# Kernel tuning notes

Measured on AMD Instinct MI355X. Metric: run time of the kernel, lower is better.

## Reference

```python
import jax, jax.numpy as jnp
from jax import lax
import numpy as np

NUM_HEADS = 8
KW = 3  # window kernel size

def _avgpool3(x):
    # x: [B,C,H,W]; AvgPool2d(3,1,1) with count_include_pad=True -> sum/9
    s = lax.reduce_window(x, 0.0, lax.add, (1, 1, KW, KW), (1, 1, 1, 1),
                          ((0, 0), (0, 0), (1, 1), (1, 1)))
    return s / (KW * KW)

def _unfold3(y):
    # y: [B,h,w,C] -> [B,h,w,9,C]; patch index ordered row-major (kh,kw)
    B, h, w, C = y.shape
    yp = jnp.pad(y, ((0, 0), (1, 1), (1, 1), (0, 0)))
    return jnp.stack([yp[:, i:i + h, j:j + w, :]
                      for i in range(KW) for j in range(KW)], axis=3)

def setup_inputs():
    key = jax.random.key(0)
    ks = jax.random.split(key, 9)
    B, C, H, W = 8, 256, 64, 64
    sd = 0.02
    return {
        "x": jax.random.normal(ks[0], (B, C, H, W), jnp.float32),
        "W_qkv": jax.random.normal(ks[1], (4 * C, C), jnp.float32) * sd,
        "b_qkv": jnp.zeros((4 * C,), jnp.float32),
        "W1": jax.random.normal(ks[2], (C // 2, C), jnp.float32) * sd,
        "b1": jnp.zeros((C // 2,), jnp.float32),
        "W2": jax.random.normal(ks[3], (C, C // 2), jnp.float32) * sd,
        "b2": jnp.zeros((C,), jnp.float32),
        "Wp": jax.random.normal(ks[4], (C, C), jnp.float32) * sd,
        "bp": jnp.zeros((C,), jnp.float32),
    }

def reference(x, W_qkv, b_qkv, W1, b1, W2, b2, Wp, bp):
    B, C, H, W = x.shape
    nH = NUM_HEADS
    hd = C // nH
    scale = hd ** -0.5
    # avg pool (stride 1 keeps spatial dims), to channels-last
    y = _avgpool3(x).transpose(0, 2, 3, 1)                 # [B,h,w,C]
    qkv = y @ W_qkv.T + b_qkv                              # [B,h,w,4C]
    qkv = qkv.reshape(B, H, W, C, 4)
    q, k, v, chans = qkv[..., 0], qkv[..., 1], qkv[..., 2], qkv[..., 3]
    # channel gate
    g = jax.nn.sigmoid(jax.nn.relu(chans @ W1.T + b1) @ W2.T + b2)  # [B,h,w,C]
    # local window attention: each query attends to its 3x3 neighborhood
    qh = q.reshape(B, H, W, nH, hd)                        # [B,h,w,n,d]
    kp = _unfold3(k).reshape(B, H, W, KW * KW, nH, hd)     # [B,h,w,9,n,d]
    vp = _unfold3(v).reshape(B, H, W, KW * KW, nH, hd)
    attn = jnp.einsum('bhwnd,bhwknd->bhwnk', qh, kp) * scale
    attn = jax.nn.softmax(attn, axis=-1)
    out = jnp.einsum('bhwnk,bhwknd->bhwnd', attn, vp).reshape(B, H, W, C)
    out = out * g + out
    out = out @ Wp.T + bp
    return out.transpose(0, 3, 1, 2)                       # [B,C,H,W]
```

## Files before the change

### kernel.cpp

```cpp
#include <hip/hip_runtime.h>
#include <stdint.h>

typedef __bf16    bf16x8 __attribute__((ext_vector_type(8)));
typedef float     f32x4  __attribute__((ext_vector_type(4)));
typedef uint32_t  u32x4  __attribute__((ext_vector_type(4)));
typedef uint32_t  u32x2  __attribute__((ext_vector_type(2)));

#define MFMA(a,b,c) __builtin_amdgcn_mfma_f32_16x16x32_bf16((a),(b),(c),0,0,0)

__device__ __align__(16) uint16_t g_y [8*64*64*256];
__device__ __align__(16) uint16_t g_wpk[393216];

#define WQF 0
#define WKF 65536
#define WVF 131072
#define WCF 196608
#define W1F 262144
#define W2F 294912
#define WPF 327680

static __device__ __forceinline__ float b2f(uint32_t u){ return __builtin_bit_cast(float, u<<16); }
static __device__ __forceinline__ uint32_t f2b(float f){
  uint32_t x = __builtin_bit_cast(uint32_t, f);
  return (x + 0x7fffu + ((x>>16)&1u)) >> 16;
}

__global__ __launch_bounds__(512) void kprep(const float* __restrict__ x,
    const float* __restrict__ Wqkv, const float* __restrict__ W1,
    const float* __restrict__ W2, const float* __restrict__ Wp){
  int t = threadIdx.x;
  int bid = blockIdx.x;
  if (bid < 1024){
    __shared__ __align__(16) uint16_t sm[3*128*82];
    uint32_t* smw = (uint32_t*)sm;
    int b = bid >> 7, h = (bid >> 1) & 63, ch = (bid & 1) << 7;
    for (int i=t; i<384; i+=512){
      int base = i*41;
      smw[base+3]  = 0;
      smw[base+36] = 0;
    }
    if (h==0 || h==63){
      int hh = (h==0) ? 0 : 2;
      for (int i=t; i<5248; i+=512) smw[hh*5248 + i] = 0;
    }
    #pragma unroll
    for (int i=0;i<12;i++){
      int id = t + 512*i;
      int w4 = id&15, c = (id>>4)&127, hh = id>>11;
      int gy = h - 1 + hh;
      if ((unsigned)gy < 64u){
        f32x4 ld = *(const f32x4*)&x[(((b*256+ch+c)*64+gy)*64) + w4*4];
        int wb = (((hh*128+c)*82 + 8 + w4*4) >> 1);
        smw[wb+0] = f2b(ld[0]) | (f2b(ld[1])<<16);
        smw[wb+1] = f2b(ld[2]) | (f2b(ld[3])<<16);
      }
    }
    __syncthreads();
    int c = t & 127, wsel = t >> 7;
    int r0 = c*82, r1 = r0 + 128*82, r2 = r1 + 128*82;
    int w0 = wsel*16;
    float csp = b2f(sm[r0+w0+7]) + b2f(sm[r1+w0+7]) + b2f(sm[r2+w0+7]);
    float csc = b2f(sm[r0+w0+8]) + b2f(sm[r1+w0+8]) + b2f(sm[r2+w0+8]);
    uint16_t* dst = g_y + ((b*64+h)*64)*256 + ch + c;
    for (int j2=0;j2<16;j2++){
      int w = w0 + j2;
      float csn = b2f(sm[r0+w+9]) + b2f(sm[r1+w+9]) + b2f(sm[r2+w+9]);
      float yv = (csp + csc + csn) * (1.0f/9.0f);
      dst[w*256] = (uint16_t)f2b(yv);
      csp = csc; csc = csn;
    }
  } else {
    int idx = (bid - 1024)*512 + t;
    int j = idx & 7, lane = (idx>>3)&63;
    int n16 = lane & 15, q4 = lane>>4;
    float v;
    if (idx < 262144){
      int tt = idx >> 16, l = idx & 65535;
      int s = (l>>9)&7, nt = l>>12;
      v = Wqkv[(4*(nt*16+n16) + tt)*256 + s*32 + q4*8 + j];
    } else if (idx < 294912){
      int l = idx - 262144;
      int s = (l>>9)&7, nt = l>>12;
      v = W1[(nt*16+n16)*256 + s*32 + q4*8 + j];
    } else if (idx < 327680){
      int l = idx - 294912;
      int s = (l>>9)&3, nt = l>>11;
      v = W2[(nt*16+n16)*128 + s*32 + q4*8 + j];
    } else {
      int l = idx - 327680;
      int s = (l>>9)&7, nt = l>>12;
      v = Wp[(nt*16+n16)*256 + s*32 + q4*8 + j];
    }
    g_wpk[idx] = (uint16_t)f2b(v);
  }
}

#define YSTR  264
#define HSTR  136
#define K2_QS 15840
#define K2_KS 20192
#define K2_VS 28352
#define MCH   0
#define MHS   8448
#define MAO   15840
#define MAOSTR 266
#define MAOT  15840
#define MTSTR 36
__global__ __launch_bounds__(512,4) void kattn(const float* __restrict__ bqkv,
    const float* __restrict__ b1, const float* __restrict__ b2v,
    const float* __restrict__ bp, float* __restrict__ out){
  __shared__ __align__(16) uint16_t sm[36512];
  int t = threadIdx.x;
  int lane = t & 63, wave = t >> 6;
  int n16 = lane & 15, quad = lane >> 4;
  int bid = blockIdx.x;
  int bb = bid >> 7, ty = (bid >> 3) & 15, tx = bid & 7;

  uint32_t opk[2][8];
  uint32_t chp[16];

  #pragma unroll
  for (int i=0;i<4;i++){
    int id = t + 512*i;
    if (id < 1920){
      int hp = id >> 5, c8 = id & 31;
      int py = hp/10, px = hp - py*10;
      int gy = ty*4 + py - 1, gx = tx*8 + px - 1;
      u32x4 ld = {0,0,0,0};
      if ((unsigned)gy<64u && (unsigned)gx<64u)
        ld = *(const u32x4*)&g_y[((bb*64+gy)*64+gx)*256 + c8*8];
      *(u32x4*)&sm[hp*YSTR + c8*8] = ld;
    }
  }
  __syncthreads();

  #pragma unroll
  for (int hf=0; hf<2; hf++){
    {
      int ntg = hf*8 + wave;
      bf16x8 Bq[8];
      #pragma unroll
      for (int s=0;s<8;s++) Bq[s] = *(const bf16x8*)&g_wpk[WQF + ((ntg*8+s)*64+lane)*8];
      float bq = bqkv[4*(ntg*16+n16) + 0];
      int colB = wave*16;
      #pragma unroll
      for (int mt=0; mt<2; mt++){
        f32x4 a = {0.f,0.f,0.f,0.f};
        int m = mt*16 + n16;
        int hrow = 10*(m>>3) + (m&7) + 11;
        #pragma unroll
        for (int s=0;s<8;s++){
          bf16x8 A = *(const bf16x8*)&sm[hrow*YSTR + s*32 + quad*8];
          a = MFMA(A, Bq[s], a);
        }
        #pragma unroll
        for (int r=0;r<4;r++){
          int row = mt*16 + quad*4 + r;
          sm[K2_QS + row*HSTR + colB + n16] = (uint16_t)f2b(a[r] + bq);
        }
      }
    }
    __syncthreads();
    {
      int ntg = hf*8 + wave;
      bf16x8 Bk[8], Bv[8];
      #pragma unroll
      for (int s=0;s<8;s++){
        Bk[s] = *(const bf16x8*)&g_wpk[WKF + ((ntg*8+s)*64+lane)*8];
        Bv[s] = *(const bf16x8*)&g_wpk[WVF + ((ntg*8+s)*64+lane)*8];
      }
      float bk = bqkv[4*(ntg*16+n16) + 1];
      float bv = bqkv[4*(ntg*16+n16) + 2];
      int colB = wave*16;
      #pragma unroll
      for (int mt=0; mt<4; mt++){
        f32x4 ak = {0.f,0.f,0.f,0.f}, av = {0.f,0.f,0.f,0.f};
        int m = mt*16 + n16;
        int mr = (m < 60) ? m : 59;
        #pragma unroll
        for (int s=0;s<8;s++){
          bf16x8 A = *(const bf16x8*)&sm[mr*YSTR + s*32 + quad*8];
          ak = MFMA(A, Bk[s], ak);
          av = MFMA(A, Bv[s], av);
        }
        #pragma unroll
        for (int r=0;r<4;r++){
          int row = mt*16 + quad*4 + r;
          if (row < 60){
            int py = row/10, px = row - py*10;
            int gy = ty*4 + py - 1, gx = tx*8 + px - 1;
            bool ok = ((unsigned)gy<64u) && ((unsigned)gx<64u);
            float vk = ok ? ak[r] + bk : 0.f;
            float vv = ok ? av[r] + bv : 0.f;
            sm[K2_KS + row*HSTR + colB + n16] = (uint16_t)f2b(vk);
            sm[K2_VS + row*HSTR + colB + n16] = (uint16_t)f2b(vv);
          }
        }
      }
    }
    __syncthreads();
    if (wave < 4){
      int p = lane & 31, half = lane >> 5;
      int cb = wave*32 + half*16;
      const uint16_t* qp = &sm[K2_QS + p*HSTR + cb];
      u32x4 qa = *(const u32x4*)qp;
      u32x4 qb = *(const u32x4*)(qp+8);
      float qv[16];
      #pragma unroll
      for (int i=0;i<4;i++){
        qv[2*i]    = b2f(qa[i]&0xffffu); qv[2*i+1]   = b2f(qa[i]>>16);
        qv[8+2*i]  = b2f(qb[i]&0xffffu); qv[8+2*i+1] = b2f(qb[i]>>16);
      }
      int hb = 10*(p>>3) + (p&7) + 11;
      const int off[9] = {-11,-10,-9,-1,0,1,9,10,11};
      float sc[9];
      #pragma unroll
      for (int nb=0;nb<9;nb++){
        const uint16_t* kp = &sm[K2_KS + (hb+off[nb])*HSTR + cb];
        u32x4 ka = *(const u32x4*)kp;
        u32x4 kb = *(const u32x4*)(kp+8);
        float s = 0.f;
        #pragma unroll
        for (int i=0;i<4;i++){
          s += qv[2*i]*b2f(ka[i]&0xffffu)   + qv[2*i+1]*b2f(ka[i]>>16);
          s += qv[8+2*i]*b2f(kb[i]&0xffffu) + qv[8+2*i+1]*b2f(kb[i]>>16);
        }
        s += __shfl_xor(s, 32);
        sc[nb] = s * 0.17677669529663687f;
      }
      float mx = sc[0];
      #pragma unroll
      for (int nb=1;nb<9;nb++) mx = fmaxf(mx, sc[nb]);
      float l = 0.f;
      #pragma unroll
      for (int nb=0;nb<9;nb++){ sc[nb] = __expf(sc[nb]-mx); l += sc[nb]; }
      float inv = 1.f / l;
      float o[16];
      #pragma unroll
      for (int i=0;i<16;i++) o[i]=0.f;
      #pragma unroll
      for (int nb=0;nb<9;nb++){
        float wgt = sc[nb]*inv;
        const uint16_t* vp = &sm[K2_VS + (hb+off[nb])*HSTR + cb];
        u32x4 va = *(const u32x4*)vp;
        u32x4 vb = *(const u32x4*)(vp+8);
        #pragma unroll
        for (int i=0;i<4;i++){
          o[2*i]    += wgt*b2f(va[i]&0xffffu); o[2*i+1]   += wgt*b2f(va[i]>>16);
          o[8+2*i]  += wgt*b2f(vb[i]&0xffffu); o[8+2*i+1] += wgt*b2f(vb[i]>>16);
        }
      }
      #pragma unroll
      for (int i=0;i<8;i++) opk[hf][i] = f2b(o[2*i]) | (f2b(o[2*i+1])<<16);
    } else if (hf == 0){
      #pragma unroll
      for (int jj=0;jj<4;jj++){
        int ntg = (wave-4)*4 + jj;
        bf16x8 Bc[8];
        #pragma unroll
        for (int s=0;s<8;s++) Bc[s] = *(const bf16x8*)&g_wpk[WCF + ((ntg*8+s)*64+lane)*8];
        float bc = bqkv[4*(ntg*16+n16) + 3];
        #pragma unroll
        for (int mt=0; mt<2; mt++){
          f32x4 a = {0.f,0.f,0.f,0.f};
          int m = mt*16 + n16;
          int hrow = 10*(m>>3) + (m&7) + 11;
          #pragma unroll
          for (int s=0;s<8;s++){
            bf16x8 A = *(const bf16x8*)&sm[hrow*YSTR + s*32 + quad*8];
            a = MFMA(A, Bc[s], a);
          }
          chp[(jj*2+mt)*2+0] = f2b(a[0]+bc) | (f2b(a[1]+bc)<<16);
          chp[(jj*2+mt)*2+1] = f2b(a[2]+bc) | (f2b(a[3]+bc)<<16);
        }
      }
    } else {
      #pragma unroll
      for (int jj=0;jj<4;jj++){
        int ntg = (wave-4)*4 + jj;
        int col = ntg*16 + n16;
        #pragma unroll
        for (int mt=0;mt<2;mt++){
          #pragma unroll
          for (int r2=0;r2<2;r2++){
            uint32_t v = chp[(jj*2+mt)*2+r2];
            int row = mt*16 + quad*4 + r2*2;
            sm[MCH + row*264 + col]     = (uint16_t)(v & 0xffffu);
            sm[MCH + (row+1)*264 + col] = (uint16_t)(v >> 16);
          }
        }
      }
    }
    __syncthreads();
  }
  if (wave < 4){
    int p = lane & 31, half = lane >> 5;
    int cb = wave*32 + half*16;
    #pragma unroll
    for (int hf=0;hf<2;hf++)
      #pragma unroll
      for (int i=0;i<8;i++)
        *(uint32_t*)&sm[MAO + p*MAOSTR + hf*128 + cb + 2*i] = opk[hf][i];
  }
  {
    int ntg = wave;
    bf16x8 Bf[8];
    #pragma unroll
    for (int s=0;s<8;s++) Bf[s] = *(const bf16x8*)&g_wpk[W1F + ((ntg*8+s)*64+lane)*8];
    float bs = b1[ntg*16+n16];
    int colB = wave*16;
    #pragma unroll
    for (int mt=0;mt<2;mt++){
      f32x4 a = {0.f,0.f,0.f,0.f};
      #pragma unroll
      for (int s=0;s<8;s++){
        bf16x8 A = *(const bf16x8*)&sm[MCH + (mt*16+n16)*264 + s*32 + quad*8];
        a = MFMA(A, Bf[s], a);
      }
      #pragma unroll
      for (int r=0;r<4;r++){
        int row = mt*16 + quad*4 + r;
        sm[MHS + row*HSTR + colB + n16] = (uint16_t)f2b(fmaxf(a[r]+bs, 0.f));
      }
    }
  }
  __syncthreads();
  #pragma unroll
  for (int jj=0;jj<2;jj++){
    int ntg = wave*2 + jj;
    bf16x8 Bf[4];
    #pragma unroll
    for (int s=0;s<4;s++) Bf[s] = *(const bf16x8*)&g_wpk[W2F + ((ntg*4+s)*64+lane)*8];
    float bs = b2v[ntg*16+n16];
    int colB = ntg*16;
    #pragma unroll
    for (int mt=0;mt<2;mt++){
      f32x4 a = {0.f,0.f,0.f,0.f};
      #pragma unroll
      for (int s=0;s<4;s++){
        bf16x8 A = *(const bf16x8*)&sm[MHS + (mt*16+n16)*HSTR + s*32 + quad*8];
        a = MFMA(A, Bf[s], a);
      }
      #pragma unroll
      for (int r=0;r<4;r++){
        int row = mt*16 + quad*4 + r;
        float gg = 1.f/(1.f+__expf(-(a[r] + bs)));
        float ao = b2f((uint32_t)sm[MAO + row*MAOSTR + colB + n16]);
        sm[MCH + row*264 + colB + n16] = (uint16_t)f2b(ao*(1.f+gg));
      }
    }
  }
  __syncthreads();
  #pragma unroll
  for (int jj=0;jj<2;jj++){
    int ntg = wave*2 + jj;
    bf16x8 Bf[8];
    #pragma unroll
    for (int s=0;s<8;s++) Bf[s] = *(const bf16x8*)&g_wpk[WPF + ((ntg*8+s)*64+lane)*8];
    float bs = bp[ntg*16+n16];
    int colB = ntg*16;
    #pragma unroll
    for (int mt=0;mt<2;mt++){
      f32x4 a = {0.f,0.f,0.f,0.f};
      #pragma unroll
      for (int s=0;s<8;s++){
        bf16x8 A = *(const bf16x8*)&sm[MCH + (mt*16+n16)*264 + s*32 + quad*8];
        a = MFMA(A, Bf[s], a);
      }
      uint32_t lo = f2b(a[0]+bs) | (f2b(a[1]+bs)<<16);
      uint32_t hi = f2b(a[2]+bs) | (f2b(a[3]+bs)<<16);
      int col = colB + n16, row0 = mt*16 + quad*4;
      u32x2 pk = {lo, hi};
      *(u32x2*)&sm[MAOT + col*MTSTR + row0] = pk;
    }
  }
  __syncthreads();
  #pragma unroll
  for (int i=0;i<4;i++){
    int idx = t + 512*i;
    int ix4 = idx&1, iy = (idx>>1)&3, c = idx>>3;
    int p0 = iy*8 + ix4*4;
    u32x2 pk = *(const u32x2*)&sm[MAOT + c*MTSTR + p0];
    f32x4 stv;
    stv[0] = b2f(pk[0]&0xffffu); stv[1] = b2f(pk[0]>>16);
    stv[2] = b2f(pk[1]&0xffffu); stv[3] = b2f(pk[1]>>16);
    *(f32x4*)&out[(((bb*256+c)*64) + ty*4+iy)*64 + tx*8 + ix4*4] = stv;
  }
}

extern "C" void kernel_launch(void* const* d_in, const int* in_sizes, int n_in,
                              void* d_out, int out_size, void* d_ws, size_t ws_size,
                              hipStream_t stream){
  (void)in_sizes; (void)n_in; (void)d_ws; (void)ws_size; (void)out_size;
  const float* x    = (const float*)d_in[0];
  const float* Wqkv = (const float*)d_in[1];
  const float* bqkv = (const float*)d_in[2];
  const float* W1   = (const float*)d_in[3];
  const float* b1   = (const float*)d_in[4];
  const float* W2   = (const float*)d_in[5];
  const float* b2   = (const float*)d_in[6];
  const float* Wp   = (const float*)d_in[7];
  const float* bp   = (const float*)d_in[8];
  kprep<<<dim3(1792), dim3(512), 0, stream>>>(x, Wqkv, W1, W2, Wp);
  kattn<<<dim3(1024), dim3(512), 0, stream>>>(bqkv, b1, b2, bp, (float*)d_out);
}
```

Before: 186.1 us.

## Rebalance attention kernel schedule so waves overlap Q projection with attention

Restructures the fused attention kernel. All waves now compute the first-half Q and the channel-gate projection together up front. Waves 4-7 then compute the second-half Q into a separate buffer while waves 0-3 run the first attention pass, and the second attention pass overlaps with the channel scatter into shared memory. The conversion to bf16 now uses the native __bf16 cast, and bf16 unpacking uses a mask instead of a shift. The W2 and Wp GEMMs are restructured to reuse their A fragments across two output tiles. Shared memory grows to hold a second Q buffer, which may reduce occupancy, and the idle-wave imbalance in the attention phase is reduced.

```diff
diff --git a/kernel.cpp b/kernel.cpp
--- a/kernel.cpp
+++ b/kernel.cpp
@@ -20,9 +20,13 @@
 #define WPF 327680
 
 static __device__ __forceinline__ float b2f(uint32_t u){ return __builtin_bit_cast(float, u<<16); }
-static __device__ __forceinline__ uint32_t f2b(float f){
-  uint32_t x = __builtin_bit_cast(uint32_t, f);
-  return (x + 0x7fffu + ((x>>16)&1u)) >> 16;
+static __device__ __forceinline__ float blo(uint32_t u){ return __builtin_bit_cast(float, u<<16); }
+static __device__ __forceinline__ float bhi(uint32_t u){ return __builtin_bit_cast(float, u & 0xffff0000u); }
+static __device__ __forceinline__ uint16_t f2bn(float f){
+  return __builtin_bit_cast(uint16_t, (__bf16)f);
+}
+static __device__ __forceinline__ uint32_t pk2(float x, float y){
+  return (uint32_t)f2bn(x) | ((uint32_t)f2bn(y) << 16);
 }
 
 __global__ __launch_bounds__(512) void kprep(const float* __restrict__ x,
@@ -51,8 +55,8 @@
       if ((unsigned)gy < 64u){
         f32x4 ld = *(const f32x4*)&x[(((b*256+ch+c)*64+gy)*64) + w4*4];
         int wb = (((hh*128+c)*82 + 8 + w4*4) >> 1);
-        smw[wb+0] = f2b(ld[0]) | (f2b(ld[1])<<16);
-        smw[wb+1] = f2b(ld[2]) | (f2b(ld[3])<<16);
+        smw[wb+0] = pk2(ld[0], ld[1]);
+        smw[wb+1] = pk2(ld[2], ld[3]);
       }
     }
     __syncthreads();
@@ -66,7 +70,7 @@
       int w = w0 + j2;
       float csn = b2f(sm[r0+w+9]) + b2f(sm[r1+w+9]) + b2f(sm[r2+w+9]);
       float yv = (csp + csc + csn) * (1.0f/9.0f);
-      dst[w*256] = (uint16_t)f2b(yv);
+      dst[w*256] = f2bn(yv);
       csp = csc; csc = csn;
     }
   } else {
@@ -91,33 +95,94 @@
       int s = (l>>9)&7, nt = l>>12;
       v = Wp[(nt*16+n16)*256 + s*32 + q4*8 + j];
     }
-    g_wpk[idx] = (uint16_t)f2b(v);
+    g_wpk[idx] = f2bn(v);
   }
 }
 
 #define YSTR  264
+#define QA    15840
+#define QB    20192
+#define KS    24544
+#define VS    32704
 #define HSTR  136
-#define K2_QS 15840
-#define K2_KS 20192
-#define K2_VS 28352
 #define MCH   0
 #define MHS   8448
 #define MAO   15840
 #define MAOSTR 266
 #define MAOT  15840
 #define MTSTR 36
+
+static __device__ __forceinline__ void attn_pass(const uint16_t* sm, int qbase,
+    int lane, int wave, uint32_t* opk){
+  int p = lane & 31, half = lane >> 5;
+  int cb = wave*32 + half*16;
+  const uint16_t* qp = &sm[qbase + p*HSTR + cb];
+  u32x4 qa = *(const u32x4*)qp;
+  u32x4 qb = *(const u32x4*)(qp+8);
+  float qv[16];
+  #pragma unroll
+  for (int i=0;i<4;i++){
+    qv[2*i]    = blo(qa[i]); qv[2*i+1]   = bhi(qa[i]);
+    qv[8+2*i]  = blo(qb[i]); qv[8+2*i+1] = bhi(qb[i]);
+  }
+  int hb = 10*(p>>3) + (p&7) + 11;
+  const int off[9] = {-11,-10,-9,-1,0,1,9,10,11};
+  float sc[9];
+  #pragma unroll
+  for (int nb=0;nb<9;nb++){
+    const uint16_t* kp = &sm[KS + (hb+off[nb])*HSTR + cb];
+    u32x4 ka = *(const u32x4*)kp;
+    u32x4 kb = *(const u32x4*)(kp+8);
+    float s = 0.f;
+    #pragma unroll
+    for (int i=0;i<4;i++){
+      s += qv[2*i]*blo(ka[i])   + qv[2*i+1]*bhi(ka[i]);
+      s += qv[8+2*i]*blo(kb[i]) + qv[8+2*i+1]*bhi(kb[i]);
+    }
+    s += __shfl_xor(s, 32);
+    sc[nb] = s * 0.17677669529663687f;
+  }
+  float mx = sc[0];
+  #pragma unroll
+  for (int nb=1;nb<9;nb++) mx = fmaxf(mx, sc[nb]);
+  float l = 0.f;
+  #pragma unroll
+  for (int nb=0;nb<9;nb++){ sc[nb] = __expf(sc[nb]-mx); l += sc[nb]; }
+  float inv = 1.f / l;
+  float o[16];
+  #pragma unroll
+  for (int i=0;i<16;i++) o[i]=0.f;
+  #pragma unroll
+  for (int nb=0;nb<9;nb++){
+    float wgt = sc[nb]*inv;
+    const uint16_t* vp = &sm[VS + (hb+off[nb])*HSTR + cb];
+    u32x4 va = *(const u32x4*)vp;
+    u32x4 vb = *(const u32x4*)(vp+8);
+    #pragma unroll
+    for (int i=0;i<4;i++){
+      o[2*i]    += wgt*blo(va[i]); o[2*i+1]   += wgt*bhi(va[i]);
+      o[8+2*i]  += wgt*blo(vb[i]); o[8+2*i+1] += wgt*bhi(vb[i]);
+    }
+  }
+  #pragma unroll
+  for (int i=0;i<8;i++) opk[i] = pk2(o[2*i], o[2*i+1]);
+}
+
 __global__ __launch_bounds__(512,4) void kattn(const float* __restrict__ bqkv,
     const float* __restrict__ b1, const float* __restrict__ b2v,
     const float* __restrict__ bp, float* __restrict__ out){
-  __shared__ __align__(16) uint16_t sm[36512];
+  __shared__ __align__(16) uint16_t sm[40864];
   int t = threadIdx.x;
   int lane = t & 63, wave = t >> 6;
   int n16 = lane & 15, quad = lane >> 4;
   int bid = blockIdx.x;
   int bb = bid >> 7, ty = (bid >> 3) & 15, tx = bid & 7;
 
-  uint32_t opk[2][8];
-  uint32_t chp[16];
+  uint32_t opk0[8], opk1[8];
+  uint32_t chp[8];
+
+  int hrow0 = 10*(n16>>3) + (n16&7) + 11;
+  int hrow1 = hrow0 + 20;
 
   #pragma unroll
   for (int i=0;i<4;i++){
@@ -134,247 +199,250 @@
   }
   __syncthreads();
 
-  #pragma unroll
-  for (int hf=0; hf<2; hf++){
-    {
-      int ntg = hf*8 + wave;
-      bf16x8 Bq[8];
-      #pragma unroll
-      for (int s=0;s<8;s++) Bq[s] = *(const bf16x8*)&g_wpk[WQF + ((ntg*8+s)*64+lane)*8];
-      float bq = bqkv[4*(ntg*16+n16) + 0];
-      int colB = wave*16;
-      #pragma unroll
-      for (int mt=0; mt<2; mt++){
-        f32x4 a = {0.f,0.f,0.f,0.f};
-        int m = mt*16 + n16;
-        int hrow = 10*(m>>3) + (m&7) + 11;
-        #pragma unroll
-        for (int s=0;s<8;s++){
-          bf16x8 A = *(const bf16x8*)&sm[hrow*YSTR + s*32 + quad*8];
-          a = MFMA(A, Bq[s], a);
+  {
+    int ntgQ = wave, ntC0 = wave*2, ntC1 = wave*2+1;
+    f32x4 aq0={0.f,0.f,0.f,0.f}, aq1={0.f,0.f,0.f,0.f};
+    f32x4 c00={0.f,0.f,0.f,0.f}, c01={0.f,0.f,0.f,0.f};
+    f32x4 c10={0.f,0.f,0.f,0.f}, c11={0.f,0.f,0.f,0.f};
+    #pragma unroll
+    for (int s=0;s<8;s++){
+      bf16x8 Bq  = *(const bf16x8*)&g_wpk[WQF + ((ntgQ*8+s)*64+lane)*8];
+      bf16x8 Bc0 = *(const bf16x8*)&g_wpk[WCF + ((ntC0*8+s)*64+lane)*8];
+      bf16x8 Bc1 = *(const bf16x8*)&g_wpk[WCF + ((ntC1*8+s)*64+lane)*8];
+      bf16x8 A0 = *(const bf16x8*)&sm[hrow0*YSTR + s*32 + quad*8];
+      bf16x8 A1 = *(const bf16x8*)&sm[hrow1*YSTR + s*32 + quad*8];
+      aq0 = MFMA(A0,Bq,aq0);  aq1 = MFMA(A1,Bq,aq1);
+      c00 = MFMA(A0,Bc0,c00); c01 = MFMA(A1,Bc0,c01);
+      c10 = MFMA(A0,Bc1,c10); c11 = MFMA(A1,Bc1,c11);
+    }
+    float bq  = bqkv[4*(ntgQ*16+n16) + 0];
+    float bc0 = bqkv[4*(ntC0*16+n16) + 3];
+    float bc1 = bqkv[4*(ntC1*16+n16) + 3];
+    int colB = wave*16;
+    #pragma unroll
+    for (int r=0;r<4;r++){
+      sm[QA + (quad*4+r)*HSTR + colB + n16]      = f2bn(aq0[r]+bq);
+      sm[QA + (16+quad*4+r)*HSTR + colB + n16]   = f2bn(aq1[r]+bq);
+    }
+    chp[0] = pk2(c00[0]+bc0, c00[1]+bc0); chp[1] = pk2(c00[2]+bc0, c00[3]+bc0);
+    chp[2] = pk2(c01[0]+bc0, c01[1]+bc0); chp[3] = pk2(c01[2]+bc0, c01[3]+bc0);
+    chp[4] = pk2(c10[0]+bc1, c10[1]+bc1); chp[5] = pk2(c10[2]+bc1, c10[3]+bc1);
+    chp[6] = pk2(c11[0]+bc1, c11[1]+bc1); chp[7] = pk2(c11[2]+bc1, c11[3]+bc1);
+  }
+  {
+    int ntg = wave;
+    bf16x8 Bk[8], Bv[8];
+    #pragma unroll
+    for (int s=0;s<8;s++){
+      Bk[s] = *(const bf16x8*)&g_wpk[WKF + ((ntg*8+s)*64+lane)*8];
+      Bv[s] = *(const bf16x8*)&g_wpk[WVF + ((ntg*8+s)*64+lane)*8];
+    }
+    float bk = bqkv[4*(ntg*16+n16) + 1];
+    float bv = bqkv[4*(ntg*16+n16) + 2];
+    int colB = wave*16;
+    #pragma unroll
+    for (int mt=0; mt<4; mt++){
+      f32x4 ak = {0.f,0.f,0.f,0.f}, av = {0.f,0.f,0.f,0.f};
+      int m = mt*16 + n16;
+      int mr = (m < 60) ? m : 59;
+      #pragma unroll
+      for (int s=0;s<8;s++){
+        bf16x8 A = *(const bf16x8*)&sm[mr*YSTR + s*32 + quad*8];
+        ak = MFMA(A, Bk[s], ak);
+        av = MFMA(A, Bv[s], av);
+      }
+      #pragma unroll
+      for (int r=0;r<4;r++){
+        int row = mt*16 + quad*4 + r;
+        if (row < 60){
+          int py = row/10, px = row - py*10;
+          int gy = ty*4 + py - 1, gx = tx*8 + px - 1;
+          bool ok = ((unsigned)gy<64u) && ((unsigned)gx<64u);
+          sm[KS + row*HSTR + colB + n16] = ok ? f2bn(ak[r] + bk) : (uint16_t)0;
+          sm[VS + row*HSTR + colB + n16] = ok ? f2bn(av[r] + bv) : (uint16_t)0;
         }
+      }
+    }
+  }
+  __syncthreads();
+
+  if (wave < 4){
+    attn_pass(sm, QA, lane, wave, opk0);
+  } else {
+    int nt0 = 8 + (wave-4)*2, nt1 = nt0 + 1;
+    f32x4 a00={0.f,0.f,0.f,0.f}, a01={0.f,0.f,0.f,0.f};
+    f32x4 a10={0.f,0.f,0.f,0.f}, a11={0.f,0.f,0.f,0.f};
+    #pragma unroll
+    for (int s=0;s<8;s++){
+      bf16x8 B0 = *(const bf16x8*)&g_wpk[WQF + ((nt0*8+s)*64+lane)*8];
+      bf16x8 B1 = *(const bf16x8*)&g_wpk[WQF + ((nt1*8+s)*64+lane)*8];
+      bf16x8 A0 = *(const bf16x8*)&sm[hrow0*YSTR + s*32 + quad*8];
+      bf16x8 A1 = *(const bf16x8*)&sm[hrow1*YSTR + s*32 + quad*8];
+      a00 = MFMA(A0,B0,a00); a01 = MFMA(A1,B0,a01);
+      a10 = MFMA(A0,B1,a10); a11 = MFMA(A1,B1,a11);
+    }
+    float bq0 = bqkv[4*(nt0*16+n16) + 0];
+    float bq1 = bqkv[4*(nt1*16+n16) + 0];
+    int c0 = (nt0-8)*16, c1 = (nt1-8)*16;
+    #pragma unroll
+    for (int r=0;r<4;r++){
+      sm[QB + (quad*4+r)*HSTR + c0 + n16]    = f2bn(a00[r]+bq0);
+      sm[QB + (16+quad*4+r)*HSTR + c0 + n16] = f2bn(a01[r]+bq0);
+      sm[QB + (quad*4+r)*HSTR + c1 + n16]    = f2bn(a10[r]+bq1);
+      sm[QB + (16+quad*4+r)*HSTR + c1 + n16] = f2bn(a11[r]+bq1);
+    }
+  }
+  __syncthreads();
+
+  {
+    int ntg = 8 + wave;
+    bf16x8 Bk[8], Bv[8];
+    #pragma unroll
+    for (int s=0;s<8;s++){
+      Bk[s] = *(const bf16x8*)&g_wpk[WKF + ((ntg*8+s)*64+lane)*8];
+      Bv[s] = *(const bf16x8*)&g_wpk[WVF + ((ntg*8+s)*64+lane)*8];
+    }
+    float bk = bqkv[4*(ntg*16+n16) + 1];
+    float bv = bqkv[4*(ntg*16+n16) + 2];
+    int colB = wave*16;
+    #pragma unroll
+    for (int mt=0; mt<4; mt++){
+      f32x4 ak = {0.f,0.f,0.f,0.f}, av = {0.f,0.f,0.f,0.f};
+      int m = mt*16 + n16;
+      int mr = (m < 60) ? m : 59;
+      #pragma unroll
+      for (int s=0;s<8;s++){
+        bf16x8 A = *(const bf16x8*)&sm[mr*YSTR + s*32 + quad*8];
+        ak = MFMA(A, Bk[s], ak);
+        av = MFMA(A, Bv[s], av);
+      }
+      #pragma unroll
+      for (int r=0;r<4;r++){
+        int row = mt*16 + quad*4 + r;
+        if (row < 60){
+          int py = row/10, px = row - py*10;
+          int gy = ty*4 + py - 1, gx = tx*8 + px - 1;
+          bool ok = ((unsigned)gy<64u) && ((unsigned)gx<64u);
+          sm[KS + row*HSTR + colB + n16] = ok ? f2bn(ak[r] + bk) : (uint16_t)0;
+          sm[VS + row*HSTR + colB + n16] = ok ? f2bn(av[r] + bv) : (uint16_t)0;
+        }
+      }
+    }
+  }
+  __syncthreads();
+
+  #pragma unroll
+  for (int jj=0;jj<2;jj++){
+    int col = (wave*2+jj)*16 + n16;
+    #pragma unroll
+    for (int mt=0;mt<2;mt++){
+      #pragma unroll
+      for (int r2=0;r2<2;r2++){
+        uint32_t v = chp[(jj*2+mt)*2+r2];
+        int row = mt*16 + quad*4 + r2*2;
+        sm[MCH + row*264 + col]     = (uint16_t)(v & 0xffffu);
+        sm[MCH + (row+1)*264 + col] = (uint16_t)(v >> 16);
+      }
+    }
+  }
+  if (wave < 4) attn_pass(sm, QB, lane, wave, opk1);
+  __syncthreads();
+
+  if (wave < 4){
+    int p = lane & 31, half = lane >> 5;
+    int cb = wave*32 + half*16;
+    #pragma unroll
+    for (int i=0;i<8;i++){
+      *(uint32_t*)&sm[MAO + p*MAOSTR + cb + 2*i]       = opk0[i];
+      *(uint32_t*)&sm[MAO + p*MAOSTR + 128 + cb + 2*i] = opk1[i];
+    }
+  }
+  {
+    int ntg = wave;
+    bf16x8 Bf[8];
+    #pragma unroll
+    for (int s=0;s<8;s++) Bf[s] = *(const bf16x8*)&g_wpk[W1F + ((ntg*8+s)*64+lane)*8];
+    float bs = b1[ntg*16+n16];
+    int colB = wave*16;
+    #pragma unroll
+    for (int mt=0;mt<2;mt++){
+      f32x4 a = {0.f,0.f,0.f,0.f};
+      #pragma unroll
+      for (int s=0;s<8;s++){
+        bf16x8 A = *(const bf16x8*)&sm[MCH + (mt*16+n16)*264 + s*32 + quad*8];
+        a = MFMA(A, Bf[s], a);
+      }
+      #pragma unroll
+      for (int r=0;r<4;r++){
+        int row = mt*16 + quad*4 + r;
+        sm[MHS + row*HSTR + colB + n16] = f2bn(fmaxf(a[r]+bs, 0.f));
+      }
+    }
+  }
+  __syncthreads();
+
+  {
+    int nt0 = wave*2, nt1 = nt0+1;
+    f32x4 g00={0.f,0.f,0.f,0.f}, g01={0.f,0.f,0.f,0.f};
+    f32x4 g10={0.f,0.f,0.f,0.f}, g11={0.f,0.f,0.f,0.f};
+    #pragma unroll
+    for (int s=0;s<4;s++){
+      bf16x8 B0 = *(const bf16x8*)&g_wpk[W2F + ((nt0*4+s)*64+lane)*8];
+      bf16x8 B1 = *(const bf16x8*)&g_wpk[W2F + ((nt1*4+s)*64+lane)*8];
+      bf16x8 A0 = *(const bf16x8*)&sm[MHS + n16*HSTR + s*32 + quad*8];
+      bf16x8 A1 = *(const bf16x8*)&sm[MHS + (16+n16)*HSTR + s*32 + quad*8];
+      g00 = MFMA(A0,B0,g00); g01 = MFMA(A1,B0,g01);
+      g10 = MFMA(A0,B1,g10); g11 = MFMA(A1,B1,g11);
+    }
+    float bs0 = b2v[nt0*16+n16], bs1 = b2v[nt1*16+n16];
+    #pragma unroll
+    for (int jj=0;jj<2;jj++){
+      int colB = (wave*2+jj)*16;
+      float bs = jj ? bs1 : bs0;
+      #pragma unroll
+      for (int mt=0;mt<2;mt++){
+        f32x4 a = jj ? (mt ? g11 : g10) : (mt ? g01 : g00);
         #pragma unroll
         for (int r=0;r<4;r++){
           int row = mt*16 + quad*4 + r;
-          sm[K2_QS + row*HSTR + colB + n16] = (uint16_t)f2b(a[r] + bq);
+          float gg = 1.f/(1.f+__expf(-(a[r] + bs)));
+          float ao = b2f((uint32_t)sm[MAO + row*MAOSTR + colB + n16]);
+          sm[MCH + row*264 + colB + n16] = f2bn(ao*(1.f+gg));
         }
       }
     }
-    __syncthreads();
-    {
-      int ntg = hf*8 + wave;
-      bf16x8 Bk[8], Bv[8];
-      #pragma unroll
-      for (int s=0;s<8;s++){
-        Bk[s] = *(const bf16x8*)&g_wpk[WKF + ((ntg*8+s)*64+lane)*8];
-        Bv[s] = *(const bf16x8*)&g_wpk[WVF + ((ntg*8+s)*64+lane)*8];
-      }
-      float bk = bqkv[4*(ntg*16+n16) + 1];
-      float bv = bqkv[4*(ntg*16+n16) + 2];
-      int colB = wave*16;
-      #pragma unroll
-      for (int mt=0; mt<4; mt++){
-        f32x4 ak = {0.f,0.f,0.f,0.f}, av = {0.f,0.f,0.f,0.f};
-        int m = mt*16 + n16;
-        int mr = (m < 60) ? m : 59;
-        #pragma unroll
-        for (int s=0;s<8;s++){
-          bf16x8 A = *(const bf16x8*)&sm[mr*YSTR + s*32 + quad*8];
-          ak = MFMA(A, Bk[s], ak);
-          av = MFMA(A, Bv[s], av);
-        }
-        #pragma unroll
-        for (int r=0;r<4;r++){
-          int row = mt*16 + quad*4 + r;
-          if (row < 60){
-            int py = row/10, px = row - py*10;
-            int gy = ty*4 + py - 1, gx = tx*8 + px - 1;
-            bool ok = ((unsigned)gy<64u) && ((unsigned)gx<64u);
-            float vk = ok ? ak[r] + bk : 0.f;
-            float vv = ok ? av[r] + bv : 0.f;
-            sm[K2_KS + row*HSTR + colB + n16] = (uint16_t)f2b(vk);
-            sm[K2_VS + row*HSTR + colB + n16] = (uint16_t)f2b(vv);
-          }
-        }
-      }
-    }
-    __syncthreads();
-    if (wave < 4){
-      int p = lane & 31, half = lane >> 5;
-      int cb = wave*32 + half*16;
-      const uint16_t* qp = &sm[K2_QS + p*HSTR + cb];
-      u32x4 qa = *(const u32x4*)qp;
-      u32x4 qb = *(const u32x4*)(qp+8);
-      float qv[16];
-      #pragma unroll
-      for (int i=0;i<4;i++){
-        qv[2*i]    = b2f(qa[i]&0xffffu); qv[2*i+1]   = b2f(qa[i]>>16);
-        qv[8+2*i]  = b2f(qb[i]&0xffffu); qv[8+2*i+1] = b2f(qb[i]>>16);
-      }
-      int hb = 10*(p>>3) + (p&7) + 11;
-      const int off[9] = {-11,-10,-9,-1,0,1,9,10,11};
-      float sc[9];
-      #pragma unroll
-      for (int nb=0;nb<9;nb++){
-        const uint16_t* kp = &sm[K2_KS + (hb+off[nb])*HSTR + cb];
-        u32x4 ka = *(const u32x4*)kp;
-        u32x4 kb = *(const u32x4*)(kp+8);
-        float s = 0.f;
-        #pragma unroll
-        for (int i=0;i<4;i++){
-          s += qv[2*i]*b2f(ka[i]&0xffffu)   + qv[2*i+1]*b2f(ka[i]>>16);
-          s += qv[8+2*i]*b2f(kb[i]&0xffffu) + qv[8+2*i+1]*b2f(kb[i]>>16);
-        }
-        s += __shfl_xor(s, 32);
-        sc[nb] = s * 0.17677669529663687f;
-      }
-      float mx = sc[0];
-      #pragma unroll
-      for (int nb=1;nb<9;nb++) mx = fmaxf(mx, sc[nb]);
-      float l = 0.f;
-      #pragma unroll
-      for (int nb=0;nb<9;nb++){ sc[nb] = __expf(sc[nb]-mx); l += sc[nb]; }
-      float inv = 1.f / l;
-      float o[16];
-      #pragma unroll
-      for (int i=0;i<16;i++) o[i]=0.f;
-      #pragma unroll
-      for (int nb=0;nb<9;nb++){
-        float wgt = sc[nb]*inv;
-        const uint16_t* vp = &sm[K2_VS + (hb+off[nb])*HSTR + cb];
-        u32x4 va = *(const u32x4*)vp;
-        u32x4 vb = *(const u32x4*)(vp+8);
-        #pragma unroll
-        for (int i=0;i<4;i++){
-          o[2*i]    += wgt*b2f(va[i]&0xffffu); o[2*i+1]   += wgt*b2f(va[i]>>16);
-          o[8+2*i]  += wgt*b2f(vb[i]&0xffffu); o[8+2*i+1] += wgt*b2f(vb[i]>>16);
-        }
-      }
-      #pragma unroll
-      for (int i=0;i<8;i++) opk[hf][i] = f2b(o[2*i]) | (f2b(o[2*i+1])<<16);
-    } else if (hf == 0){
-      #pragma unroll
-      for (int jj=0;jj<4;jj++){
-        int ntg = (wave-4)*4 + jj;
-        bf16x8 Bc[8];
-        #pragma unroll
-        for (int s=0;s<8;s++) Bc[s] = *(const bf16x8*)&g_wpk[WCF + ((ntg*8+s)*64+lane)*8];
-        float bc = bqkv[4*(ntg*16+n16) + 3];
-        #pragma unroll
-        for (int mt=0; mt<2; mt++){
-          f32x4 a = {0.f,0.f,0.f,0.f};
-          int m = mt*16 + n16;
-          int hrow = 10*(m>>3) + (m&7) + 11;
-          #pragma unroll
-          for (int s=0;s<8;s++){
-            bf16x8 A = *(const bf16x8*)&sm[hrow*YSTR + s*32 + quad*8];
-            a = MFMA(A, Bc[s], a);
-          }
-          chp[(jj*2+mt)*2+0] = f2b(a[0]+bc) | (f2b(a[1]+bc)<<16);
-          chp[(jj*2+mt)*2+1] = f2b(a[2]+bc) | (f2b(a[3]+bc)<<16);
-        }
-      }
-    } else {
-      #pragma unroll
-      for (int jj=0;jj<4;jj++){
-        int ntg = (wave-4)*4 + jj;
-        int col = ntg*16 + n16;
-        #pragma unroll
-        for (int mt=0;mt<2;mt++){
-          #pragma unroll
-          for (int r2=0;r2<2;r2++){
-            uint32_t v = chp[(jj*2+mt)*2+r2];
-            int row = mt*16 + quad*4 + r2*2;
-            sm[MCH + row*264 + col]     = (uint16_t)(v & 0xffffu);
-            sm[MCH + (row+1)*264 + col] = (uint16_t)(v >> 16);
-          }
-        }
-      }
-    }
-    __syncthreads();
-  }
-  if (wave < 4){
-    int p = lane & 31, half = lane >> 5;
-    int cb = wave*32 + half*16;
-    #pragma unroll
-    for (int hf=0;hf<2;hf++)
-      #pragma unroll
-      for (int i=0;i<8;i++)
-        *(uint32_t*)&sm[MAO + p*MAOSTR + hf*128 + cb + 2*i] = opk[hf][i];
-  }
-  {
-    int ntg = wave;
-    bf16x8 Bf[8];
-    #pragma unroll
-    for (int s=0;s<8;s++) Bf[s] = *(const bf16x8*)&g_wpk[W1F + ((ntg*8+s)*64+lane)*8];
-    float bs = b1[ntg*16+n16];
-    int colB = wave*16;
-    #pragma unroll
-    for (int mt=0;mt<2;mt++){
-      f32x4 a = {0.f,0.f,0.f,0.f};
-      #pragma unroll
-      for (int s=0;s<8;s++){
-        bf16x8 A = *(const bf16x8*)&sm[MCH + (mt*16+n16)*264 + s*32 + quad*8];
-        a = MFMA(A, Bf[s], a);
-      }
-      #pragma unroll
-      for (int r=0;r<4;r++){
-        int row = mt*16 + quad*4 + r;
-        sm[MHS + row*HSTR + colB + n16] = (uint16_t)f2b(fmaxf(a[r]+bs, 0.f));
-      }
-    }
-  }
-  __syncthreads();
-  #pragma unroll
-  for (int jj=0;jj<2;jj++){
-    int ntg = wave*2 + jj;
-    bf16x8 Bf[4];
-    #pragma unroll
-    for (int s=0;s<4;s++) Bf[s] = *(const bf16x8*)&g_wpk[W2F + ((ntg*4+s)*64+lane)*8];
-    float bs = b2v[ntg*16+n16];
-    int colB = ntg*16;
-    #pragma unroll
-    for (int mt=0;mt<2;mt++){
-      f32x4 a = {0.f,0.f,0.f,0.f};
-      #pragma unroll
-      for (int s=0;s<4;s++){
-        bf16x8 A = *(const bf16x8*)&sm[MHS + (mt*16+n16)*HSTR + s*32 + quad*8];
-        a = MFMA(A, Bf[s], a);
-      }
-      #pragma unroll
-      for (int r=0;r<4;r++){
-        int row = mt*16 + quad*4 + r;
-        float gg = 1.f/(1.f+__expf(-(a[r] + bs)));
-        float ao = b2f((uint32_t)sm[MAO + row*MAOSTR + colB + n16]);
-        sm[MCH + row*264 + colB + n16] = (uint16_t)f2b(ao*(1.f+gg));
-      }
-    }
-  }
-  __syncthreads();
-  #pragma unroll
-  for (int jj=0;jj<2;jj++){
-    int ntg = wave*2 + jj;
-    bf16x8 Bf[8];
-    #pragma unroll
-    for (int s=0;s<8;s++) Bf[s] = *(const bf16x8*)&g_wpk[WPF + ((ntg*8+s)*64+lane)*8];
-    float bs = bp[ntg*16+n16];
-    int colB = ntg*16;
-    #pragma unroll
-    for (int mt=0;mt<2;mt++){
-      f32x4 a = {0.f,0.f,0.f,0.f};
-      #pragma unroll
-      for (int s=0;s<8;s++){
-        bf16x8 A = *(const bf16x8*)&sm[MCH + (mt*16+n16)*264 + s*32 + quad*8];
-        a = MFMA(A, Bf[s], a);
-      }
-      uint32_t lo = f2b(a[0]+bs) | (f2b(a[1]+bs)<<16);
-      uint32_t hi = f2b(a[2]+bs) | (f2b(a[3]+bs)<<16);
-      int col = colB + n16, row0 = mt*16 + quad*4;
-      u32x2 pk = {lo, hi};
-      *(u32x2*)&sm[MAOT + col*MTSTR + row0] = pk;
-    }
-  }
-  __syncthreads();
+  }
+  __syncthreads();
+
+  {
+    int nt0 = wave*2, nt1 = nt0+1;
+    f32x4 p00={0.f,0.f,0.f,0.f}, p01={0.f,0.f,0.f,0.f};
+    f32x4 p10={0.f,0.f,0.f,0.f}, p11={0.f,0.f,0.f,0.f};
+    #pragma unroll
+    for (int s=0;s<8;s++){
+      bf16x8 B0 = *(const bf16x8*)&g_wpk[WPF + ((nt0*8+s)*64+lane)*8];
+      bf16x8 B1 = *(const bf16x8*)&g_wpk[WPF + ((nt1*8+s)*64+lane)*8];
+      bf16x8 A0 = *(const bf16x8*)&sm[MCH + n16*264 + s*32 + quad*8];
+      bf16x8 A1 = *(const bf16x8*)&sm[MCH + (16+n16)*264 + s*32 + quad*8];
+      p00 = MFMA(A0,B0,p00); p01 = MFMA(A1,B0,p01);
+      p10 = MFMA(A0,B1,p10); p11 = MFMA(A1,B1,p11);
+    }
+    float bs0 = bp[nt0*16+n16], bs1 = bp[nt1*16+n16];
+    #pragma unroll
+    for (int jj=0;jj<2;jj++){
+      int col = (wave*2+jj)*16 + n16;
+      float bs = jj ? bs1 : bs0;
+      #pragma unroll
+      for (int mt=0;mt<2;mt++){
+        f32x4 a = jj ? (mt ? p11 : p10) : (mt ? p01 : p00);
+        u32x2 pk = { pk2(a[0]+bs, a[1]+bs), pk2(a[2]+bs, a[3]+bs) };
+        int row0 = mt*16 + quad*4;
+        *(u32x2*)&sm[MAOT + col*MTSTR + row0] = pk;
+      }
+    }
+  }
+  __syncthreads();
+
   #pragma unroll
   for (int i=0;i<4;i++){
     int idx = t + 512*i;
@@ -382,8 +450,8 @@
     int p0 = iy*8 + ix4*4;
     u32x2 pk = *(const u32x2*)&sm[MAOT + c*MTSTR + p0];
     f32x4 stv;
-    stv[0] = b2f(pk[0]&0xffffu); stv[1] = b2f(pk[0]>>16);
-    stv[2] = b2f(pk[1]&0xffffu); stv[3] = b2f(pk[1]>>16);
+    stv[0] = blo(pk[0]); stv[1] = bhi(pk[0]);
+    stv[2] = blo(pk[1]); stv[3] = bhi(pk[1]);
     *(f32x4*)&out[(((bb*256+c)*64) + ty*4+iy)*64 + tx*8 + ix4*4] = stv;
   }
 }
```

Result: no change. 188.5 us (+1.3%).
